# Performance work log

Hardware: AMD Instinct MI355X
Metric: run time of the kernel (lower is better)

## Reference

```python
import jax, jax.numpy as jnp
import numpy as np

B, T, C = 4, 2048, 1024
H = 16
D = C // H  # 64


def setup_inputs() -> dict:
    key = jax.random.key(0)
    k1, k2, k3 = jax.random.split(key, 3)
    x = jax.random.normal(k1, (B, T, C), dtype=jnp.float32)
    w_qkv = jax.random.normal(k2, (C, 3 * C), dtype=jnp.float32) * (C ** -0.5)
    b_qkv = jnp.zeros((3 * C,), dtype=jnp.float32)
    w_proj = jax.random.normal(k3, (C, C), dtype=jnp.float32) * (C ** -0.5)
    b_proj = jnp.zeros((C,), dtype=jnp.float32)
    return {"x": x, "w_qkv": w_qkv, "b_qkv": b_qkv, "w_proj": w_proj, "b_proj": b_proj}


def reference(x, w_qkv, b_qkv, w_proj, b_proj):
    qkv = x @ w_qkv + b_qkv                      # [B,T,3C]
    q, k, v = jnp.split(qkv, 3, axis=-1)
    # [B,T,C] -> [B,H,T,D]
    q = q.reshape(B, T, H, D).transpose(0, 2, 1, 3)
    k = k.reshape(B, T, H, D).transpose(0, 2, 1, 3)
    v = v.reshape(B, T, H, D).transpose(0, 2, 1, 3)
    scale = 1.0 / jnp.sqrt(jnp.float32(D))
    att = jnp.einsum('bhqd,bhkd->bhqk', q, k) * scale  # [B,H,T,T]
    causal = jnp.tril(jnp.ones((T, T), dtype=bool))
    att = jnp.where(causal[None, None], att, -jnp.inf)
    att = jax.nn.softmax(att, axis=-1)
    y = jnp.einsum('bhqk,bhkd->bhqd', att, v)          # [B,H,T,D]
    y = y.transpose(0, 2, 1, 3).reshape(B, T, C)
    return y @ w_proj + b_proj
```

## Files before the change

### kernel.cpp

```cpp
#include <hip/hip_runtime.h>
#include <hip/hip_bf16.h>
#include <stdint.h>

#define B_ 4
#define T_ 2048
#define C_ 1024
#define H_ 16
#define D_ 64

typedef __bf16 bf16;
typedef _Float16 f16;
typedef __attribute__((ext_vector_type(8))) __bf16 bf16x8;
typedef __attribute__((ext_vector_type(4))) __bf16 bf16x4;
typedef __attribute__((ext_vector_type(4))) _Float16 f16x4;
typedef __attribute__((ext_vector_type(8))) _Float16 f16x8;
typedef __attribute__((ext_vector_type(4))) float floatx4;

__device__ __forceinline__ floatx4 mfma16(bf16x8 a, bf16x8 b, floatx4 c) {
  return __builtin_amdgcn_mfma_f32_16x16x32_bf16(a, b, c, 0, 0, 0);
}
__device__ __forceinline__ floatx4 mfma_pv(f16x4 a, f16x4 b, floatx4 c) {
  return __builtin_amdgcn_mfma_f32_16x16x16f16(a, b, c, 0, 0, 0);
}

__device__ __forceinline__ void gl_lds16(const void* g, void* l) {
  __builtin_amdgcn_global_load_lds(
      (__attribute__((address_space(1))) uint32_t*)g,
      (__attribute__((address_space(3))) uint32_t*)l, 16, 0, 0);
}

__global__ __launch_bounds__(256) void cvt_bf16(const float* __restrict__ in,
                                                bf16* __restrict__ out) {
  const size_t i = ((size_t)blockIdx.x * 256 + threadIdx.x) * 4;
  const floatx4 v = *(const floatx4*)(in + i);
  bf16x4 r;
#pragma unroll
  for (int j = 0; j < 4; j++) r[j] = (bf16)v[j];
  *(bf16x4*)(out + i) = r;
}

__global__ __launch_bounds__(256) void transpose_f32(const float* __restrict__ in,
                                                     bf16* __restrict__ out,
                                                     int K, int N) {
  __shared__ bf16 tile[32][33];
  const int n0 = blockIdx.x * 32, k0 = blockIdx.y * 32;
  const int r = threadIdx.x >> 5, c = threadIdx.x & 31;
#pragma unroll
  for (int i = 0; i < 4; i++)
    tile[r + i * 8][c] = (bf16)in[(size_t)(k0 + r + i * 8) * N + n0 + c];
  __syncthreads();
#pragma unroll
  for (int i = 0; i < 4; i++)
    out[(size_t)(n0 + r + i * 8) * K + k0 + c] = tile[c][r + i * 8];
}

template <int MODE>
__global__ __launch_bounds__(256) void gemm128(const bf16* __restrict__ A,
                                               const bf16* __restrict__ Bt,
                                               const float* __restrict__ bias,
                                               void* __restrict__ o0,
                                               bf16* __restrict__ o1,
                                               f16* __restrict__ o2,
                                               int M, int N, int K) {
  __shared__ __align__(16) bf16 As[2][128 * 32];
  __shared__ __align__(16) bf16 Bs[2][128 * 32];
  const int tid = threadIdx.x;
  const int m0 = blockIdx.y * 128, n0 = blockIdx.x * 128;
  const int lane = tid & 63, wv = tid >> 6;
  const int wm = (wv >> 1) * 64, wn = (wv & 1) * 64;
  const int col = lane & 15, quad = lane >> 4;

  floatx4 acc[4][4];
#pragma unroll
  for (int i = 0; i < 4; i++)
#pragma unroll
    for (int j = 0; j < 4; j++) acc[i][j] = (floatx4){0.f, 0.f, 0.f, 0.f};

  const int c0 = tid, c1 = tid + 256;
  const bf16* a0 = A + (size_t)(m0 + (c0 >> 2)) * K + (c0 & 3) * 8;
  const bf16* a1 = A + (size_t)(m0 + (c1 >> 2)) * K + (c1 & 3) * 8;
  const bf16* b0 = Bt + (size_t)(n0 + (c0 >> 2)) * K + (c0 & 3) * 8;
  const bf16* b1 = Bt + (size_t)(n0 + (c1 >> 2)) * K + (c1 & 3) * 8;

  for (int kt = 0; kt < K; kt += 64) {
#pragma unroll
    for (int hf = 0; hf < 2; hf++) {
      const int ko = kt + hf * 32;
      gl_lds16(a0 + ko, &As[hf][(wv * 64) * 8]);
      gl_lds16(a1 + ko, &As[hf][(wv * 64 + 256) * 8]);
      gl_lds16(b0 + ko, &Bs[hf][(wv * 64) * 8]);
      gl_lds16(b1 + ko, &Bs[hf][(wv * 64 + 256) * 8]);
    }
    __syncthreads();
#pragma unroll
    for (int hf = 0; hf < 2; hf++) {
      bf16x8 afr[4], bg[4];
#pragma unroll
      for (int mb = 0; mb < 4; mb++)
        afr[mb] = *(const bf16x8*)&As[hf][(wm + mb * 16 + col) * 32 + quad * 8];
#pragma unroll
      for (int nb = 0; nb < 4; nb++)
        bg[nb] = *(const bf16x8*)&Bs[hf][(wn + nb * 16 + col) * 32 + quad * 8];
#pragma unroll
      for (int mb = 0; mb < 4; mb++)
#pragma unroll
        for (int nb = 0; nb < 4; nb++)
          acc[mb][nb] = mfma16(afr[mb], bg[nb], acc[mb][nb]);
    }
    __syncthreads();
  }

#pragma unroll
  for (int mb = 0; mb < 4; mb++) {
    const int mgq = m0 + wm + mb * 16 + quad * 4;
    if (MODE == 0) {
      const int third = mgq >> 10;
      const int nn0 = mgq & 1023;
      const int h = nn0 >> 6, d0 = nn0 & 63;
      float bs[4];
#pragma unroll
      for (int r = 0; r < 4; r++) bs[r] = bias[mgq + r];
#pragma unroll
      for (int nb = 0; nb < 4; nb++) {
        const int t = n0 + wn + nb * 16 + col;
        const int bb = t >> 11, tt = t & 2047;
        const size_t bh = (size_t)bb * H_ + h;
        float v[4];
#pragma unroll
        for (int r = 0; r < 4; r++) v[r] = acc[mb][nb][r] + bs[r];
        if (third == 0) {
          bf16x4 y;
#pragma unroll
          for (int r = 0; r < 4; r++) y[r] = (bf16)v[r];
          *(bf16x4*)&((bf16*)o0)[(bh * T_ + tt) * D_ + d0] = y;
        } else if (third == 1) {
          const int lane2 = (tt & 15) | (((d0 >> 3) & 3) << 4);
          const size_t idx =
              ((((bh * 64 + (tt >> 5)) * 2 + ((tt >> 4) & 1)) * 2 + (d0 >> 5)) * 64 +
               lane2) * 8 + (d0 & 7);
          bf16x4 y;
#pragma unroll
          for (int r = 0; r < 4; r++) y[r] = (bf16)v[r];
          *(bf16x4*)&o1[idx] = y;
        } else {
#pragma unroll
          for (int r = 0; r < 4; r++) {
            const int d = d0 + r;
            const int lane2 = (d & 15) | (((tt >> 2) & 3) << 4);
            const size_t idx =
                (((bh * 64 + (tt >> 5)) * 4 + (d >> 4)) * 64 + lane2) * 8 +
                ((tt >> 4) & 1) * 4 + (tt & 3);
            o2[idx] = (f16)v[r];
          }
        }
      }
    } else {
#pragma unroll
      for (int nb = 0; nb < 4; nb++) {
        const int ng = n0 + wn + nb * 16 + col;
        const float bsc = bias[ng];
#pragma unroll
        for (int r = 0; r < 4; r++)
          ((float*)o0)[(size_t)(mgq + r) * N + ng] = acc[mb][nb][r] + bsc;
      }
    }
  }
}

__global__ __launch_bounds__(256, 4) void attn(const bf16* __restrict__ Q,
                                               const bf16* __restrict__ Kp,
                                               const f16* __restrict__ Vp,
                                               bf16* __restrict__ Y) {
  const int tid = threadIdx.x, lane = tid & 63, wv = tid >> 6;
  const int col = lane & 15, quad = lane >> 4;
  const int id = blockIdx.x;
  const int j = id >> 3;
  const int bh = ((j & 7) << 3) | (id & 7);
  const int qtile = 63 - (j >> 3);
  const int b = bh >> 4, h = bh & 15;
  const int qbase = qtile * 32;

  __shared__ __align__(16) floatx4 mbuf[3][8][64];
  __shared__ float lbuf[3][2][64];

  bf16x8 qf[2][2];
#pragma unroll
  for (int mq = 0; mq < 2; mq++) {
    const bf16* qp = Q + ((size_t)bh * T_ + qbase + mq * 16 + col) * D_ + quad * 8;
    qf[mq][0] = *(const bf16x8*)qp;
    qf[mq][1] = *(const bf16x8*)(qp + 32);
  }

  floatx4 o[2][4];
  float lsum[2] = {0.f, 0.f};
#pragma unroll
  for (int mq = 0; mq < 2; mq++)
#pragma unroll
    for (int s = 0; s < 4; s++) o[mq][s] = (floatx4){0.f, 0.f, 0.f, 0.f};

  const float C1 = 0.18033688f;
  const float C2 = 11.541560f;

  const int nmine = (qtile >= wv) ? ((qtile - wv) >> 2) + 1 : 0;

  for (int i = 0; i < nmine; i++) {
    const int kt = wv + 4 * i;
    const bool masked = (kt == qtile);
    const bf16* kbase = Kp + ((size_t)bh * 64 + kt) * 2048 + lane * 8;
    const f16* vbase = Vp + ((size_t)bh * 64 + kt) * 2048 + lane * 8;
    bf16x8 ka[2][2];
    ka[0][0] = *(const bf16x8*)(kbase);
    ka[0][1] = *(const bf16x8*)(kbase + 512);
    ka[1][0] = *(const bf16x8*)(kbase + 1024);
    ka[1][1] = *(const bf16x8*)(kbase + 1536);
    f16x8 vv[4];
#pragma unroll
    for (int sub = 0; sub < 4; sub++) vv[sub] = *(const f16x8*)(vbase + sub * 512);

#pragma unroll
    for (int st = 0; st < 2; st++) {
#pragma unroll
      for (int mq = 0; mq < 2; mq++) {
        if (masked && mq == 0 && st == 1) continue;
        floatx4 s = (floatx4){0.f, 0.f, 0.f, 0.f};
        s = mfma16(ka[st][0], qf[mq][0], s);
        s = mfma16(ka[st][1], qf[mq][1], s);
        f16x4 pf;
        float ps = 0.f;
        const bool diag = masked && (mq == st);
#pragma unroll
        for (int r = 0; r < 4; r++) {
          float p = exp2f(fmaf(s[r], C1, -C2));
          if (diag && (quad * 4 + r > col)) p = 0.f;
          ps += p;
          pf[r] = (f16)p;
        }
        lsum[mq] += ps;
#pragma unroll
        for (int sub = 0; sub < 4; sub++) {
          f16x4 va;
#pragma unroll
          for (int jj = 0; jj < 4; jj++) va[jj] = vv[sub][st * 4 + jj];
          o[mq][sub] = mfma_pv(va, pf, o[mq][sub]);
        }
      }
    }
  }

  if (wv != 0) {
#pragma unroll
    for (int mq = 0; mq < 2; mq++) {
#pragma unroll
      for (int sub = 0; sub < 4; sub++) mbuf[wv - 1][mq * 4 + sub][lane] = o[mq][sub];
      lbuf[wv - 1][mq][lane] = lsum[mq];
    }
  }
  __syncthreads();
  if (wv == 0) {
#pragma unroll
    for (int w = 0; w < 3; w++)
#pragma unroll
      for (int mq = 0; mq < 2; mq++) {
#pragma unroll
        for (int sub = 0; sub < 4; sub++) o[mq][sub] += mbuf[w][mq * 4 + sub][lane];
        lsum[mq] += lbuf[w][mq][lane];
      }
#pragma unroll
    for (int mq = 0; mq < 2; mq++) {
      lsum[mq] += __shfl_xor(lsum[mq], 16);
      lsum[mq] += __shfl_xor(lsum[mq], 32);
      const float rinv = 1.f / lsum[mq];
      const int qrow = qbase + mq * 16 + col;
#pragma unroll
      for (int sub = 0; sub < 4; sub++) {
        bf16x4 yv;
#pragma unroll
        for (int r = 0; r < 4; r++) yv[r] = (bf16)(o[mq][sub][r] * rinv);
        *(bf16x4*)&Y[((size_t)b * T_ + qrow) * C_ + h * 64 + sub * 16 + quad * 4] = yv;
      }
    }
  }
}

extern "C" void kernel_launch(void* const* d_in, const int* in_sizes, int n_in,
                              void* d_out, int out_size, void* d_ws, size_t ws_size,
                              hipStream_t stream) {
  (void)in_sizes; (void)n_in; (void)out_size; (void)ws_size;
  const float* x      = (const float*)d_in[0];
  const float* w_qkv  = (const float*)d_in[1];
  const float* b_qkv  = (const float*)d_in[2];
  const float* w_proj = (const float*)d_in[3];
  const float* b_proj = (const float*)d_in[4];

  char* ws = (char*)d_ws;
  bf16* wqkv_t  = (bf16*)(ws);
  bf16* wproj_t = (bf16*)(ws + 6291456);
  bf16* qb      = (bf16*)(ws + 8388608);
  bf16* kbuf    = (bf16*)(ws + 25165824);
  f16*  vtbuf   = (f16*)(ws + 41943040);
  bf16* yb      = (bf16*)(ws + 58720256);
  bf16* xb      = (bf16*)(ws + 58720256);

  cvt_bf16<<<8192, 256, 0, stream>>>(x, xb);
  transpose_f32<<<dim3(96, 32), 256, 0, stream>>>(w_qkv, wqkv_t, 1024, 3072);
  transpose_f32<<<dim3(32, 32), 256, 0, stream>>>(w_proj, wproj_t, 1024, 1024);
  gemm128<0><<<dim3(64, 24), 256, 0, stream>>>(wqkv_t, xb, b_qkv, qb, kbuf, vtbuf,
                                               3072, 8192, 1024);
  attn<<<dim3(4096), 256, 0, stream>>>(qb, kbuf, vtbuf, yb);
  gemm128<1><<<dim3(8, 64), 256, 0, stream>>>(yb, wproj_t, b_proj, d_out, nullptr,
                                              nullptr, 8192, 1024, 1024);
}
```

Before: 259.9 us.

## Add dedicated 256x256 QKV GEMM with 4-stage direct-to-LDS pipeline

Replaces the generic 128x128 GEMM for the QKV projection with a specialized kernel. It uses 512 threads, 256x256 tiles and a 4-stage ring buffer in 128KB of dynamic shared memory, filled by direct global-to-LDS loads with XOR swizzling. It also adds a grid swizzle for L2 locality and interleaves MFMA phases with barriers and priority hints so loads overlap compute. The large LDS footprint limits occupancy to one block per CU and adds hand-tuned waitcnt logic that must stay consistent with the pipeline depth.

New measurement: 261.1 us. About the same (+0.4%).

```diff
diff --git a/kernel.cpp b/kernel.cpp
--- a/kernel.cpp
+++ b/kernel.cpp
@@ -52,6 +52,153 @@
 #pragma unroll
   for (int i = 0; i < 4; i++)
     out[(size_t)(n0 + r + i * 8) * K + k0 + c] = tile[c][r + i * 8];
+}
+
+__global__ __launch_bounds__(512, 2) void gemm_qkv(const bf16* __restrict__ A,
+                                                   const bf16* __restrict__ Bt,
+                                                   const float* __restrict__ bias,
+                                                   bf16* __restrict__ Qb,
+                                                   bf16* __restrict__ Kp,
+                                                   f16* __restrict__ Vp) {
+  extern __shared__ __align__(16) char smem_[];
+  const int tid = threadIdx.x;
+  const int lane = tid & 63, wv = tid >> 6;
+  const int col = lane & 15, quad = lane >> 4;
+  const int wm = wv >> 2, wn = wv & 3;
+
+  const int id0 = blockIdx.x;
+  const int sw = (id0 & 7) * 48 + (id0 >> 3);
+  const int bx = sw / 12, by = sw - bx * 12;
+  const int m0 = by * 256, n0 = bx * 256;
+
+  const int srow = tid >> 2;
+  const int schunk = tid & 3;
+  const int sx = ((schunk ^ ((srow >> 1) & 3)) << 3);
+  const bf16* baseA0 = A + (size_t)(m0 + srow) * 1024 + sx;
+  const bf16* baseA1 = baseA0 + (size_t)128 * 1024;
+  const bf16* baseB0 = Bt + (size_t)(n0 + srow) * 1024 + sx;
+  const bf16* baseB1 = baseB0 + (size_t)128 * 1024;
+  const int wvo = wv << 10;
+
+  const int fswz = col * 64 + ((quad ^ ((col >> 1) & 3)) << 4);
+  const int aoff = (wm << 13) + fswz;
+  const int boff = 16384 + (wn << 12) + fswz;
+
+  floatx4 acc[8][4];
+#pragma unroll
+  for (int i = 0; i < 8; ++i)
+#pragma unroll
+    for (int j = 0; j < 4; ++j) acc[i][j] = (floatx4){0.f, 0.f, 0.f, 0.f};
+
+#pragma unroll
+  for (int pt = 0; pt < 3; ++pt) {
+    char* sb = smem_ + (pt << 15) + wvo;
+    gl_lds16(baseA0 + pt * 32, sb);
+    gl_lds16(baseA1 + pt * 32, sb + 8192);
+    gl_lds16(baseB0 + pt * 32, sb + 16384);
+    gl_lds16(baseB1 + pt * 32, sb + 24576);
+  }
+  asm volatile("s_waitcnt vmcnt(8)" ::: "memory");
+  __builtin_amdgcn_s_barrier();
+
+  for (int t = 0; t < 32; ++t) {
+    const char* bufp = smem_ + ((t & 3) << 15);
+    const int st = t + 3;
+    char* sb = smem_ + ((st & 3) << 15) + wvo;
+    bf16x8 afr[4], bfr[4];
+#pragma unroll
+    for (int mb = 0; mb < 4; ++mb)
+      afr[mb] = *(const bf16x8*)(bufp + aoff + mb * 1024);
+#pragma unroll
+    for (int nb = 0; nb < 4; ++nb)
+      bfr[nb] = *(const bf16x8*)(bufp + boff + nb * 1024);
+    if (st < 32) {
+      gl_lds16(baseA0 + st * 32, sb);
+      gl_lds16(baseA1 + st * 32, sb + 8192);
+    }
+    __builtin_amdgcn_s_barrier();
+    __builtin_amdgcn_sched_barrier(0);
+    __builtin_amdgcn_s_setprio(1);
+#pragma unroll
+    for (int mb = 0; mb < 4; ++mb)
+#pragma unroll
+      for (int nb = 0; nb < 4; ++nb)
+        acc[mb][nb] = mfma16(afr[mb], bfr[nb], acc[mb][nb]);
+    __builtin_amdgcn_s_setprio(0);
+    __builtin_amdgcn_sched_barrier(0);
+    __builtin_amdgcn_s_barrier();
+    bf16x8 afr2[4];
+#pragma unroll
+    for (int mb = 0; mb < 4; ++mb)
+      afr2[mb] = *(const bf16x8*)(bufp + aoff + (mb + 4) * 1024);
+    if (st < 32) {
+      gl_lds16(baseB0 + st * 32, sb + 16384);
+      gl_lds16(baseB1 + st * 32, sb + 24576);
+    }
+    __builtin_amdgcn_s_barrier();
+    __builtin_amdgcn_sched_barrier(0);
+    __builtin_amdgcn_s_setprio(1);
+#pragma unroll
+    for (int mb = 0; mb < 4; ++mb)
+#pragma unroll
+      for (int nb = 0; nb < 4; ++nb)
+        acc[mb + 4][nb] = mfma16(afr2[mb], bfr[nb], acc[mb + 4][nb]);
+    __builtin_amdgcn_s_setprio(0);
+    __builtin_amdgcn_sched_barrier(0);
+    if (t < 29)
+      asm volatile("s_waitcnt vmcnt(8)" ::: "memory");
+    else if (t == 29)
+      asm volatile("s_waitcnt vmcnt(4)" ::: "memory");
+    else if (t == 30)
+      asm volatile("s_waitcnt vmcnt(0)" ::: "memory");
+    __builtin_amdgcn_s_barrier();
+  }
+
+  const int third = by >> 2;
+  const int wrow = wm * 128, wcol = wn * 64;
+#pragma unroll
+  for (int mb = 0; mb < 8; ++mb) {
+    const int mgq = m0 + wrow + mb * 16 + quad * 4;
+    const int nn0 = mgq & 1023;
+    const int h = nn0 >> 6, d0 = nn0 & 63;
+    float bs[4];
+#pragma unroll
+    for (int r = 0; r < 4; ++r) bs[r] = bias[mgq + r];
+#pragma unroll
+    for (int nb = 0; nb < 4; ++nb) {
+      const int tk = n0 + wcol + nb * 16 + col;
+      const int bb = tk >> 11, tt = tk & 2047;
+      const size_t bh = (size_t)bb * H_ + h;
+      float v[4];
+#pragma unroll
+      for (int r = 0; r < 4; ++r) v[r] = acc[mb][nb][r] + bs[r];
+      if (third == 0) {
+        bf16x4 y;
+#pragma unroll
+        for (int r = 0; r < 4; ++r) y[r] = (bf16)v[r];
+        *(bf16x4*)&Qb[(bh * T_ + tt) * D_ + d0] = y;
+      } else if (third == 1) {
+        const int lane2 = (tt & 15) | (((d0 >> 3) & 3) << 4);
+        const size_t idx =
+            ((((bh * 64 + (tt >> 5)) * 2 + ((tt >> 4) & 1)) * 2 + (d0 >> 5)) * 64 +
+             lane2) * 8 + (d0 & 7);
+        bf16x4 y;
+#pragma unroll
+        for (int r = 0; r < 4; ++r) y[r] = (bf16)v[r];
+        *(bf16x4*)&Kp[idx] = y;
+      } else {
+#pragma unroll
+        for (int r = 0; r < 4; ++r) {
+          const int d = d0 + r;
+          const int lane2 = (d & 15) | (((tt >> 2) & 3) << 4);
+          const size_t idx =
+              (((bh * 64 + (tt >> 5)) * 4 + (d >> 4)) * 64 + lane2) * 8 +
+              ((tt >> 4) & 1) * 4 + (tt & 3);
+          Vp[idx] = (f16)v[r];
+        }
+      }
+    }
+  }
 }
 
 template <int MODE>
@@ -113,48 +260,7 @@
 #pragma unroll
   for (int mb = 0; mb < 4; mb++) {
     const int mgq = m0 + wm + mb * 16 + quad * 4;
-    if (MODE == 0) {
-      const int third = mgq >> 10;
-      const int nn0 = mgq & 1023;
-      const int h = nn0 >> 6, d0 = nn0 & 63;
-      float bs[4];
-#pragma unroll
-      for (int r = 0; r < 4; r++) bs[r] = bias[mgq + r];
-#pragma unroll
-      for (int nb = 0; nb < 4; nb++) {
-        const int t = n0 + wn + nb * 16 + col;
-        const int bb = t >> 11, tt = t & 2047;
-        const size_t bh = (size_t)bb * H_ + h;
-        float v[4];
-#pragma unroll
-        for (int r = 0; r < 4; r++) v[r] = acc[mb][nb][r] + bs[r];
-        if (third == 0) {
-          bf16x4 y;
-#pragma unroll
-          for (int r = 0; r < 4; r++) y[r] = (bf16)v[r];
-          *(bf16x4*)&((bf16*)o0)[(bh * T_ + tt) * D_ + d0] = y;
-        } else if (third == 1) {
-          const int lane2 = (tt & 15) | (((d0 >> 3) & 3) << 4);
-          const size_t idx =
-              ((((bh * 64 + (tt >> 5)) * 2 + ((tt >> 4) & 1)) * 2 + (d0 >> 5)) * 64 +
-               lane2) * 8 + (d0 & 7);
-          bf16x4 y;
-#pragma unroll
-          for (int r = 0; r < 4; r++) y[r] = (bf16)v[r];
-          *(bf16x4*)&o1[idx] = y;
-        } else {
-#pragma unroll
-          for (int r = 0; r < 4; r++) {
-            const int d = d0 + r;
-            const int lane2 = (d & 15) | (((tt >> 2) & 3) << 4);
-            const size_t idx =
-                (((bh * 64 + (tt >> 5)) * 4 + (d >> 4)) * 64 + lane2) * 8 +
-                ((tt >> 4) & 1) * 4 + (tt & 3);
-            o2[idx] = (f16)v[r];
-          }
-        }
-      }
-    } else {
+    {
 #pragma unroll
       for (int nb = 0; nb < 4; nb++) {
         const int ng = n0 + wn + nb * 16 + col;
@@ -301,11 +407,18 @@
   bf16* yb      = (bf16*)(ws + 58720256);
   bf16* xb      = (bf16*)(ws + 58720256);
 
+  static bool attr_done = false;
+  if (!attr_done) {
+    hipFuncSetAttribute(reinterpret_cast<const void*>(gemm_qkv),
+                        hipFuncAttributeMaxDynamicSharedMemorySize, 131072);
+    attr_done = true;
+  }
+
   cvt_bf16<<<8192, 256, 0, stream>>>(x, xb);
   transpose_f32<<<dim3(96, 32), 256, 0, stream>>>(w_qkv, wqkv_t, 1024, 3072);
   transpose_f32<<<dim3(32, 32), 256, 0, stream>>>(w_proj, wproj_t, 1024, 1024);
-  gemm128<0><<<dim3(64, 24), 256, 0, stream>>>(wqkv_t, xb, b_qkv, qb, kbuf, vtbuf,
-                                               3072, 8192, 1024);
+  gemm_qkv<<<dim3(384), dim3(512), 131072, stream>>>(wqkv_t, xb, b_qkv, qb, kbuf,
+                                                     vtbuf);
   attn<<<dim3(4096), 256, 0, stream>>>(qb, kbuf, vtbuf, yb);
   gemm128<1><<<dim3(8, 64), 256, 0, stream>>>(yb, wproj_t, b_proj, d_out, nullptr,
                                               nullptr, 8192, 1024, 1024);
```
